# Kernel optimization log

Hardware: AMD Instinct MI355X
Metric: run time of the kernel (lower is better)

Reference implementation:

```python
import jax, jax.numpy as jnp
import numpy as np

B, H, W, C = 32, 26, 26, 768
M = 32          # attention_num
NUM_CLASSES = 200


def setup_inputs() -> dict:
    key = jax.random.key(0)
    k1, k2, k3, k4 = jax.random.split(key, 4)
    return {
        "feat_mixed6": jax.random.normal(k1, (B, H, W, C), dtype=jnp.float32),
        "feat_mixed7": jax.random.normal(k2, (B, H, W, C), dtype=jnp.float32),
        "w_attn": jax.random.normal(k3, (C, M), dtype=jnp.float32) * 0.02,
        "w_cls": jax.random.normal(k4, (M * C, NUM_CLASSES), dtype=jnp.float32) * 0.02,
    }


def reference(feat_mixed6, feat_mixed7, w_attn, w_cls):
    b, h, w, c = feat_mixed6.shape
    m = w_attn.shape[1]
    # 1x1 conv producing attention maps: (B,H,W,M)
    attention_maps = jnp.einsum("bhwc,cm->bhwm", feat_mixed7, w_attn)
    # Bilinear attention pooling: outer product over channels, then GAP over H,W.
    # Fused as a batched contraction (avoids the (B,H,W,M,C) intermediate).
    feature_matrix = jnp.einsum("bhwm,bhwc->bmc", attention_maps, feat_mixed6) / (h * w)
    # signed sqrt
    feature_matrix = jnp.sign(feature_matrix) * jnp.sqrt(jnp.abs(feature_matrix) + 1e-12)
    # l2 normalize jointly over (attention, channel) axes, tf.nn.l2_normalize semantics
    sq = jnp.sum(feature_matrix * feature_matrix, axis=(1, 2), keepdims=True)
    feature_matrix = feature_matrix * jax.lax.rsqrt(jnp.maximum(sq, 1e-12))
    embeddings = feature_matrix.reshape(b, 1, 1, m * c)
    features = embeddings * 100.0
    # 1x1 classification conv over a 1x1 spatial map == dense layer
    logits = jnp.einsum("bk,kn->bn", features.reshape(b, m * c), w_cls)
    return (logits, attention_maps, embeddings)
```

## Files before the change

### kernel.cpp

```cpp
#include <hip/hip_runtime.h>
#include <hip/hip_bf16.h>

#define Bn   32
#define HWn  676
#define Cn   768
#define Mn   32
#define NC   200
#define KT   (Mn*Cn)
#define Sn   8
#define CHUNK 85

#define LOGITS_OFF 0
#define ATTN_OFF   (Bn*NC)
#define EMB_OFF    (ATTN_OFF + Bn*HWn*Mn)

__global__ __launch_bounds__(256) void z_kernel(float* __restrict__ out,
                                                float* __restrict__ norm_acc,
                                                int zero_emb) {
    int i = blockIdx.x * 256 + threadIdx.x;
    if (i < Bn * NC) out[LOGITS_OFF + i] = 0.f;
    if (i < Bn) norm_acc[i] = 0.f;
    if (zero_emb && i < Bn * KT) out[EMB_OFF + i] = 0.f;
}

__global__ __launch_bounds__(768, 1) void f_kernel(const float* __restrict__ f6,
                                                   const float* __restrict__ f7,
                                                   const float* __restrict__ wA,
                                                   float* __restrict__ attn_out,
                                                   float* __restrict__ part,
                                                   float* __restrict__ emb_atomic,
                                                   int partial_mode) {
    __shared__ float wS[Cn * Mn];
    __shared__ float attnS[CHUNK * Mn];

    const int tid = threadIdx.x;
    const int blk = blockIdx.x;
    const int b = blk >> 3;
    const int s = blk & 7;
    const int p0 = s * CHUNK;
    const int np = min(HWn - p0, CHUNK);

    {
        const float4* src = reinterpret_cast<const float4*>(wA);
        float4* dst = reinterpret_cast<float4*>(wS);
        #pragma unroll
        for (int i = tid; i < Cn * Mn / 4; i += 768) dst[i] = src[i];
    }
    __syncthreads();

    const int m4 = tid & 7;
    const int pg = tid >> 3;
    if (pg < np) {
        const int p = p0 + pg;
        const float4* x4p = reinterpret_cast<const float4*>(f7 + ((size_t)b * HWn + p) * Cn);
        float a0 = 0.f, a1 = 0.f, a2 = 0.f, a3 = 0.f;
        #pragma unroll 4
        for (int c4 = 0; c4 < Cn / 4; ++c4) {
            float4 x = x4p[c4];
            const float* wb = &wS[c4 * 4 * Mn + m4 * 4];
            float4 w0 = *reinterpret_cast<const float4*>(wb);
            float4 w1 = *reinterpret_cast<const float4*>(wb + Mn);
            float4 w2 = *reinterpret_cast<const float4*>(wb + 2 * Mn);
            float4 w3 = *reinterpret_cast<const float4*>(wb + 3 * Mn);
            a0 += x.x * w0.x + x.y * w1.x + x.z * w2.x + x.w * w3.x;
            a1 += x.x * w0.y + x.y * w1.y + x.z * w2.y + x.w * w3.y;
            a2 += x.x * w0.z + x.y * w1.z + x.z * w2.z + x.w * w3.z;
            a3 += x.x * w0.w + x.y * w1.w + x.z * w2.w + x.w * w3.w;
        }
        float4 r; r.x = a0; r.y = a1; r.z = a2; r.w = a3;
        *reinterpret_cast<float4*>(&attnS[pg * Mn + m4 * 4]) = r;
        *reinterpret_cast<float4*>(attn_out + ((size_t)(b * HWn + p)) * Mn + m4 * 4) = r;
    }
    __syncthreads();

    float acc[Mn];
    #pragma unroll
    for (int m = 0; m < Mn; ++m) acc[m] = 0.f;

    const float* f6b = f6 + ((size_t)b * HWn + p0) * Cn + tid;
    for (int pl = 0; pl < np; ++pl) {
        float x = f6b[(size_t)pl * Cn];
        const float4* ar = reinterpret_cast<const float4*>(&attnS[pl * Mn]);
        #pragma unroll
        for (int mq = 0; mq < 8; ++mq) {
            float4 a = ar[mq];
            acc[4 * mq + 0] += a.x * x;
            acc[4 * mq + 1] += a.y * x;
            acc[4 * mq + 2] += a.z * x;
            acc[4 * mq + 3] += a.w * x;
        }
    }

    if (partial_mode) {
        float* pdst = part + ((size_t)(b * Sn + s)) * KT + tid;
        #pragma unroll
        for (int m = 0; m < Mn; ++m) pdst[m * Cn] = acc[m];
    } else {
        float* edst = emb_atomic + (size_t)b * KT + tid;
        #pragma unroll
        for (int m = 0; m < Mn; ++m) atomicAdd(edst + m * Cn, acc[m]);
    }
}

__global__ __launch_bounds__(256) void r_kernel(const float* __restrict__ part,
                                                float* __restrict__ emb,
                                                float* __restrict__ norm_acc,
                                                int partial_mode) {
    const int tid = threadIdx.x;
    const int b = blockIdx.x >> 3;
    const int mg = blockIdx.x & 7;
    float lsq = 0.f;
    #pragma unroll
    for (int r = 0; r < 12; ++r) {
        int e = r * 256 + tid;
        int ml = e / Cn;
        int c = e - ml * Cn;
        int m = mg * 4 + ml;
        size_t off = (size_t)m * Cn + c;
        float sum;
        if (partial_mode) {
            sum = 0.f;
            #pragma unroll
            for (int s2 = 0; s2 < Sn; ++s2) sum += part[((size_t)(b * Sn + s2)) * KT + off];
        } else {
            sum = emb[(size_t)b * KT + off];
        }
        float v = sum * (1.0f / (float)HWn);
        float ssq = copysignf(sqrtf(fabsf(v) + 1e-12f), v);
        emb[(size_t)b * KT + off] = ssq;
        lsq += ssq * ssq;
    }
    #pragma unroll
    for (int o = 32; o > 0; o >>= 1) lsq += __shfl_down(lsq, o, 64);
    __shared__ float rb[4];
    if ((tid & 63) == 0) rb[tid >> 6] = lsq;
    __syncthreads();
    if (tid == 0) atomicAdd(&norm_acc[b], rb[0] + rb[1] + rb[2] + rb[3]);
}

__global__ __launch_bounds__(256) void n_kernel(float* __restrict__ emb,
                                                const float* __restrict__ norm_acc) {
    const int b = blockIdx.x >> 3;
    const int g = blockIdx.x & 7;
    float scale = rsqrtf(fmaxf(norm_acc[b], 1e-12f));
    float* p = emb + (size_t)b * KT + g * 3072 + threadIdx.x;
    #pragma unroll
    for (int r = 0; r < 12; ++r) p[r * 256] *= scale;
}

__global__ __launch_bounds__(256) void l_kernel(const float* __restrict__ emb,
                                                const float* __restrict__ wC,
                                                float* __restrict__ logits) {
    __shared__ float eS[Bn * 96];
    const int tid = threadIdx.x;
    const int k0 = blockIdx.x * 96;
    for (int i = tid; i < Bn * 96; i += 256) {
        int b = i / 96;
        int k = i - b * 96;
        eS[i] = emb[(size_t)b * KT + k0 + k] * 100.0f;
    }
    __syncthreads();
    if (tid < NC) {
        float acc[Bn];
        #pragma unroll
        for (int b = 0; b < Bn; ++b) acc[b] = 0.f;
        for (int kk = 0; kk < 96; ++kk) {
            float w = wC[(size_t)(k0 + kk) * NC + tid];
            #pragma unroll
            for (int b = 0; b < Bn; ++b) acc[b] += eS[b * 96 + kk] * w;
        }
        #pragma unroll
        for (int b = 0; b < Bn; ++b) atomicAdd(&logits[b * NC + tid], acc[b]);
    }
}

extern "C" void kernel_launch(void* const* d_in, const int* in_sizes, int n_in,
                              void* d_out, int out_size, void* d_ws, size_t ws_size,
                              hipStream_t stream) {
    const float* f6 = (const float*)d_in[0];
    const float* f7 = (const float*)d_in[1];
    const float* wA = (const float*)d_in[2];
    const float* wC = (const float*)d_in[3];
    float* out = (float*)d_out;
    float* logits = out + LOGITS_OFF;
    float* attn = out + ATTN_OFF;
    float* emb = out + EMB_OFF;

    float* norm_acc = (float*)d_ws;
    float* part = (float*)((char*)d_ws + 128);
    size_t need = 128 + (size_t)Bn * Sn * KT * sizeof(float);
    int partial = (ws_size >= need) ? 1 : 0;

    z_kernel<<<3072, 256, 0, stream>>>(out, norm_acc, !partial);
    f_kernel<<<Bn * Sn, 768, 0, stream>>>(f6, f7, wA, attn, part, emb, partial);
    r_kernel<<<Bn * 8, 256, 0, stream>>>(part, emb, norm_acc, partial);
    n_kernel<<<Bn * 8, 256, 0, stream>>>(emb, norm_acc);
    l_kernel<<<KT / 96, 256, 0, stream>>>(emb, wC, logits);
}
```

Before: 109.5 us.

## Split spatial reduction into 16 chunks, read attention weights from global, vectorize reduce

The pooling kernel now splits each image's 676 positions into 16 chunks instead of 8, doubling the block count to improve occupancy. It also drops the 96KB shared-memory copy of the attention weights and reads them straight from global/L1, with each thread computing two attention channels. The reduce and normalize kernels switch to float4 accesses, and a new intermediate mode accumulates atomically into 8 partial slots. The cost is twice as many partial buffers to write and re-read, plus repeated global weight loads in the inner loop.

```diff
diff --git a/kernel.cpp b/kernel.cpp
--- a/kernel.cpp
+++ b/kernel.cpp
@@ -7,8 +7,8 @@
 #define Mn   32
 #define NC   200
 #define KT   (Mn*Cn)
-#define Sn   8
-#define CHUNK 85
+#define Sn   16
+#define CHUNK 43
 
 #define LOGITS_OFF 0
 #define ATTN_OFF   (Bn*NC)
@@ -16,60 +16,52 @@
 
 __global__ __launch_bounds__(256) void z_kernel(float* __restrict__ out,
                                                 float* __restrict__ norm_acc,
-                                                int zero_emb) {
-    int i = blockIdx.x * 256 + threadIdx.x;
-    if (i < Bn * NC) out[LOGITS_OFF + i] = 0.f;
-    if (i < Bn) norm_acc[i] = 0.f;
-    if (zero_emb && i < Bn * KT) out[EMB_OFF + i] = 0.f;
-}
-
-__global__ __launch_bounds__(768, 1) void f_kernel(const float* __restrict__ f6,
+                                                float* __restrict__ part,
+                                                int part_elems, int zero_emb) {
+    int gid = blockIdx.x * 256 + threadIdx.x;
+    int stride = gridDim.x * 256;
+    for (int i = gid; i < Bn * NC; i += stride) out[LOGITS_OFF + i] = 0.f;
+    for (int i = gid; i < Bn; i += stride) norm_acc[i] = 0.f;
+    for (int i = gid; i < part_elems; i += stride) part[i] = 0.f;
+    if (zero_emb)
+        for (int i = gid; i < Bn * KT; i += stride) out[EMB_OFF + i] = 0.f;
+}
+
+__global__ __launch_bounds__(768, 6) void f_kernel(const float* __restrict__ f6,
                                                    const float* __restrict__ f7,
                                                    const float* __restrict__ wA,
                                                    float* __restrict__ attn_out,
                                                    float* __restrict__ part,
                                                    float* __restrict__ emb_atomic,
-                                                   int partial_mode) {
-    __shared__ float wS[Cn * Mn];
-    __shared__ float attnS[CHUNK * Mn];
+                                                   int mode) {
+    __shared__ float attnS[CHUNK * Mn + 32];
 
     const int tid = threadIdx.x;
-    const int blk = blockIdx.x;
-    const int b = blk >> 3;
-    const int s = blk & 7;
+    const int b = blockIdx.x >> 4;
+    const int s = blockIdx.x & 15;
     const int p0 = s * CHUNK;
     const int np = min(HWn - p0, CHUNK);
 
-    {
-        const float4* src = reinterpret_cast<const float4*>(wA);
-        float4* dst = reinterpret_cast<float4*>(wS);
-        #pragma unroll
-        for (int i = tid; i < Cn * Mn / 4; i += 768) dst[i] = src[i];
-    }
-    __syncthreads();
-
-    const int m4 = tid & 7;
-    const int pg = tid >> 3;
+    const int mg = tid & 15;
+    const int pg = tid >> 4;
     if (pg < np) {
         const int p = p0 + pg;
         const float4* x4p = reinterpret_cast<const float4*>(f7 + ((size_t)b * HWn + p) * Cn);
-        float a0 = 0.f, a1 = 0.f, a2 = 0.f, a3 = 0.f;
+        float a0 = 0.f, a1 = 0.f;
         #pragma unroll 4
         for (int c4 = 0; c4 < Cn / 4; ++c4) {
             float4 x = x4p[c4];
-            const float* wb = &wS[c4 * 4 * Mn + m4 * 4];
-            float4 w0 = *reinterpret_cast<const float4*>(wb);
-            float4 w1 = *reinterpret_cast<const float4*>(wb + Mn);
-            float4 w2 = *reinterpret_cast<const float4*>(wb + 2 * Mn);
-            float4 w3 = *reinterpret_cast<const float4*>(wb + 3 * Mn);
+            const float* wb = wA + (size_t)c4 * 4 * Mn + mg * 2;
+            float2 w0 = *reinterpret_cast<const float2*>(wb);
+            float2 w1 = *reinterpret_cast<const float2*>(wb + Mn);
+            float2 w2 = *reinterpret_cast<const float2*>(wb + 2 * Mn);
+            float2 w3 = *reinterpret_cast<const float2*>(wb + 3 * Mn);
             a0 += x.x * w0.x + x.y * w1.x + x.z * w2.x + x.w * w3.x;
             a1 += x.x * w0.y + x.y * w1.y + x.z * w2.y + x.w * w3.y;
-            a2 += x.x * w0.z + x.y * w1.z + x.z * w2.z + x.w * w3.z;
-            a3 += x.x * w0.w + x.y * w1.w + x.z * w2.w + x.w * w3.w;
-        }
-        float4 r; r.x = a0; r.y = a1; r.z = a2; r.w = a3;
-        *reinterpret_cast<float4*>(&attnS[pg * Mn + m4 * 4]) = r;
-        *reinterpret_cast<float4*>(attn_out + ((size_t)(b * HWn + p)) * Mn + m4 * 4) = r;
+        }
+        float2 r; r.x = a0; r.y = a1;
+        *reinterpret_cast<float2*>(&attnS[pg * Mn + mg * 2]) = r;
+        *reinterpret_cast<float2*>(attn_out + ((size_t)(b * HWn + p)) * Mn + mg * 2) = r;
     }
     __syncthreads();
 
@@ -91,10 +83,14 @@
         }
     }
 
-    if (partial_mode) {
+    if (mode == 2) {
         float* pdst = part + ((size_t)(b * Sn + s)) * KT + tid;
         #pragma unroll
         for (int m = 0; m < Mn; ++m) pdst[m * Cn] = acc[m];
+    } else if (mode == 1) {
+        float* pdst = part + ((size_t)(b * 8 + (s & 7))) * KT + tid;
+        #pragma unroll
+        for (int m = 0; m < Mn; ++m) atomicAdd(pdst + m * Cn, acc[m]);
     } else {
         float* edst = emb_atomic + (size_t)b * KT + tid;
         #pragma unroll
@@ -105,30 +101,34 @@
 __global__ __launch_bounds__(256) void r_kernel(const float* __restrict__ part,
                                                 float* __restrict__ emb,
                                                 float* __restrict__ norm_acc,
-                                                int partial_mode) {
+                                                int mode) {
     const int tid = threadIdx.x;
     const int b = blockIdx.x >> 3;
-    const int mg = blockIdx.x & 7;
+    const int g = blockIdx.x & 7;
+    const int nslots = (mode == 2) ? Sn : 8;
     float lsq = 0.f;
     #pragma unroll
-    for (int r = 0; r < 12; ++r) {
-        int e = r * 256 + tid;
-        int ml = e / Cn;
-        int c = e - ml * Cn;
-        int m = mg * 4 + ml;
-        size_t off = (size_t)m * Cn + c;
-        float sum;
-        if (partial_mode) {
-            sum = 0.f;
-            #pragma unroll
-            for (int s2 = 0; s2 < Sn; ++s2) sum += part[((size_t)(b * Sn + s2)) * KT + off];
+    for (int it = 0; it < 3; ++it) {
+        size_t e = (size_t)g * 3072 + it * 1024 + tid * 4;
+        float sx = 0.f, sy = 0.f, sz = 0.f, sw = 0.f;
+        if (mode) {
+            for (int s2 = 0; s2 < nslots; ++s2) {
+                float4 p4 = *reinterpret_cast<const float4*>(
+                    part + ((size_t)(b * nslots + s2)) * KT + e);
+                sx += p4.x; sy += p4.y; sz += p4.z; sw += p4.w;
+            }
         } else {
-            sum = emb[(size_t)b * KT + off];
-        }
-        float v = sum * (1.0f / (float)HWn);
-        float ssq = copysignf(sqrtf(fabsf(v) + 1e-12f), v);
-        emb[(size_t)b * KT + off] = ssq;
-        lsq += ssq * ssq;
+            float4 p4 = *reinterpret_cast<const float4*>(emb + (size_t)b * KT + e);
+            sx = p4.x; sy = p4.y; sz = p4.z; sw = p4.w;
+        }
+        const float inv = 1.0f / (float)HWn;
+        float4 o;
+        o.x = copysignf(sqrtf(fabsf(sx * inv) + 1e-12f), sx);
+        o.y = copysignf(sqrtf(fabsf(sy * inv) + 1e-12f), sy);
+        o.z = copysignf(sqrtf(fabsf(sz * inv) + 1e-12f), sz);
+        o.w = copysignf(sqrtf(fabsf(sw * inv) + 1e-12f), sw);
+        *reinterpret_cast<float4*>(emb + (size_t)b * KT + e) = o;
+        lsq += o.x * o.x + o.y * o.y + o.z * o.z + o.w * o.w;
     }
     #pragma unroll
     for (int o = 32; o > 0; o >>= 1) lsq += __shfl_down(lsq, o, 64);
@@ -143,9 +143,13 @@
     const int b = blockIdx.x >> 3;
     const int g = blockIdx.x & 7;
     float scale = rsqrtf(fmaxf(norm_acc[b], 1e-12f));
-    float* p = emb + (size_t)b * KT + g * 3072 + threadIdx.x;
-    #pragma unroll
-    for (int r = 0; r < 12; ++r) p[r * 256] *= scale;
+    float* p = emb + (size_t)b * KT + (size_t)g * 3072 + threadIdx.x * 4;
+    #pragma unroll
+    for (int it = 0; it < 3; ++it) {
+        float4 v = *reinterpret_cast<float4*>(p + it * 1024);
+        v.x *= scale; v.y *= scale; v.z *= scale; v.w *= scale;
+        *reinterpret_cast<float4*>(p + it * 1024) = v;
+    }
 }
 
 __global__ __launch_bounds__(256) void l_kernel(const float* __restrict__ emb,
@@ -188,12 +192,15 @@
 
     float* norm_acc = (float*)d_ws;
     float* part = (float*)((char*)d_ws + 128);
-    size_t need = 128 + (size_t)Bn * Sn * KT * sizeof(float);
-    int partial = (ws_size >= need) ? 1 : 0;
-
-    z_kernel<<<3072, 256, 0, stream>>>(out, norm_acc, !partial);
-    f_kernel<<<Bn * Sn, 768, 0, stream>>>(f6, f7, wA, attn, part, emb, partial);
-    r_kernel<<<Bn * 8, 256, 0, stream>>>(part, emb, norm_acc, partial);
+
+    size_t need2 = 128 + (size_t)Bn * Sn * KT * sizeof(float);
+    size_t need1 = 128 + (size_t)Bn * 8 * KT * sizeof(float);
+    int mode = (ws_size >= need2) ? 2 : ((ws_size >= need1) ? 1 : 0);
+    int part_elems = (mode == 1) ? Bn * 8 * KT : 0;
+
+    z_kernel<<<1024, 256, 0, stream>>>(out, norm_acc, part, part_elems, mode == 0);
+    f_kernel<<<Bn * Sn, 768, 0, stream>>>(f6, f7, wA, attn, part, emb, mode);
+    r_kernel<<<Bn * 8, 256, 0, stream>>>(part, emb, norm_acc, mode);
     n_kernel<<<Bn * 8, 256, 0, stream>>>(emb, norm_acc);
     l_kernel<<<KT / 96, 256, 0, stream>>>(emb, wC, logits);
 }
```

Measured after the change: 236.8 us. +116.3%, slower.
